# Optimization experiments

Measured on AMD Instinct MI355X. Metric: run time of the kernel, lower is better.

Reference implementation:

```python
import jax, jax.numpy as jnp
import numpy as np

EMBED = 768
NH = 12          # num_heads
NL = 3           # num_levels
NP = 4           # num_points
DV = 384         # value dim = embed_dim * deform_ratio(0.5)
DH = DV // NH    # per-head value dim = 32
B = 16
LQ = 1024        # (512/16)^2 ViT tokens
SHAPES = [(64, 64), (32, 32), (16, 16)]  # 1/8, 1/16, 1/32 pyramid of 512x512
LKV = sum(h * w for h, w in SHAPES)      # 5376
EPS = 1e-6


def layer_norm(x, w, b):
    mu = jnp.mean(x, axis=-1, keepdims=True)
    var = jnp.mean((x - mu) ** 2, axis=-1, keepdims=True)
    return (x - mu) / jnp.sqrt(var + EPS) * w + b


def bilinear_sample(v, loc, H, W):
    # v: (B, NH, H*W, DH); loc: (B, Lq, NH, P, 2) normalized in [0,1]
    # Matches torch grid_sample(align_corners=False, padding_mode='zeros').
    Bv, Lq = loc.shape[0], loc.shape[1]
    x = loc[..., 0] * W - 0.5
    y = loc[..., 1] * H - 0.5
    x0 = jnp.floor(x)
    y0 = jnp.floor(y)
    dx = x - x0
    dy = y - y0
    x0i = x0.astype(jnp.int32)
    y0i = y0.astype(jnp.int32)

    def gather(xi, yi):
        valid = (xi >= 0) & (xi < W) & (yi >= 0) & (yi < H)  # (B,Lq,NH,P)
        xc = jnp.clip(xi, 0, W - 1)
        yc = jnp.clip(yi, 0, H - 1)
        lin = (yc * W + xc).transpose(0, 2, 1, 3).reshape(Bv, NH, Lq * NP)
        g = jnp.take_along_axis(v, lin[..., None], axis=2)  # (B,NH,Lq*P,DH)
        g = g.reshape(Bv, NH, Lq, NP, DH).transpose(0, 2, 1, 3, 4)  # (B,Lq,NH,P,DH)
        return g * valid[..., None].astype(g.dtype)

    g00 = gather(x0i, y0i)
    g01 = gather(x0i + 1, y0i)
    g10 = gather(x0i, y0i + 1)
    g11 = gather(x0i + 1, y0i + 1)
    w00 = ((1 - dx) * (1 - dy))[..., None]
    w01 = (dx * (1 - dy))[..., None]
    w10 = ((1 - dx) * dy)[..., None]
    w11 = (dx * dy)[..., None]
    return g00 * w00 + g01 * w01 + g10 * w10 + g11 * w11


def ms_deform_attn_core(value, shapes_list, loc, aw):
    # value: (B,LKV,NH,DH); loc: (B,Lq,NH,NL,NP,2); aw: (B,Lq,NH,NL,NP)
    Bv, Lq = loc.shape[0], loc.shape[1]
    samples = []
    idx = 0
    for l, (H, W) in enumerate(shapes_list):
        v = value[:, idx:idx + H * W].transpose(0, 2, 1, 3)  # (B,NH,HW,DH)
        idx += H * W
        samples.append(bilinear_sample(v, loc[:, :, :, l], H, W))
    s = jnp.stack(samples, axis=3)  # (B,Lq,NH,NL,NP,DH)
    o = jnp.einsum('bqhlp,bqhlpd->bqhd', aw, s)
    return o.reshape(Bv, Lq, NH * DH)


def setup_inputs() -> dict:
    key = jax.random.key(0)
    ks = jax.random.split(key, 12)

    def n(k, shape, s=0.02):
        return jax.random.normal(k, shape, jnp.float32) * s

    return {
        'q': jax.random.normal(ks[0], (B, LQ, EMBED), jnp.float32),
        'reference_points': jax.random.uniform(ks[1], (B, LQ, NL, 2), jnp.float32),
        'kv': jax.random.normal(ks[2], (B, LKV, EMBED), jnp.float32),
        'spatial_shapes': jnp.asarray(SHAPES, jnp.int32),
        'level_start_index': jnp.asarray(
            np.cumsum([0] + [h * w for h, w in SHAPES])[:-1], jnp.int32),
        'ln1_w': jnp.ones(EMBED, jnp.float32),
        'ln1_b': jnp.zeros(EMBED, jnp.float32),
        'ln2_w': jnp.ones(EMBED, jnp.float32),
        'ln2_b': jnp.zeros(EMBED, jnp.float32),
        'gamma': n(ks[3], (EMBED,), 0.1),
        'w_off': n(ks[4], (EMBED, NH * NL * NP * 2)),
        'b_off': n(ks[5], (NH * NL * NP * 2,), 0.01),
        'w_aw': n(ks[6], (EMBED, NH * NL * NP)),
        'b_aw': jnp.zeros(NH * NL * NP, jnp.float32),
        'w_val': n(ks[7], (EMBED, DV)),
        'b_val': jnp.zeros(DV, jnp.float32),
        'w_out': n(ks[8], (DV, EMBED)),
        'b_out': jnp.zeros(EMBED, jnp.float32),
    }


def reference(q, reference_points, kv, spatial_shapes, level_start_index,
              ln1_w, ln1_b, ln2_w, ln2_b, gamma,
              w_off, b_off, w_aw, b_aw, w_val, b_val, w_out, b_out):
    shapes_list = [tuple(int(v) for v in r) for r in np.asarray(spatial_shapes)]
    Bq, Lq, _ = q.shape
    qn = layer_norm(q, ln1_w, ln1_b)
    kvn = layer_norm(kv, ln2_w, ln2_b)
    value = (kvn @ w_val + b_val).reshape(Bq, -1, NH, DH)
    off = (qn @ w_off + b_off).reshape(Bq, Lq, NH, NL, NP, 2)
    aw = (qn @ w_aw + b_aw).reshape(Bq, Lq, NH, NL * NP)
    aw = jax.nn.softmax(aw, axis=-1).reshape(Bq, Lq, NH, NL, NP)
    # offset normalizer is (W_l, H_l) per level
    wh = jnp.asarray([[w, h] for (h, w) in shapes_list], q.dtype)  # (NL,2)
    loc = reference_points[:, :, None, :, None, :] + off / wh[None, None, None, :, None, :]
    attn = ms_deform_attn_core(value, shapes_list, loc, aw)
    attn = attn @ w_out + b_out
    return q + gamma * attn
```

## Files before the change

kernel.cpp:

```cpp
#include <hip/hip_runtime.h>

#define DEV __device__ __forceinline__

typedef short bf16x8 __attribute__((ext_vector_type(8)));
typedef float f32x4 __attribute__((ext_vector_type(4)));
typedef unsigned int u32;
typedef __attribute__((address_space(1))) const u32* gas_ptr;
typedef __attribute__((address_space(3))) u32* las_ptr;

DEV short f2bf(float f) {
  union { float f; unsigned u; } un; un.f = f;
  unsigned r = un.u + 0x7FFFu + ((un.u >> 16) & 1u);
  return (short)(r >> 16);
}
DEV float bf2f(unsigned short s) {
  union { unsigned u; float f; } un;
  un.u = ((unsigned)s) << 16;
  return un.f;
}
DEV void gload16(const short* g, short* l) {
  __builtin_amdgcn_global_load_lds((gas_ptr)g, (las_ptr)l, 16, 0, 0);
}
DEV float hsum4(float4 v) { return v.x + v.y + v.z + v.w; }

__global__ __launch_bounds__(256) void pack_weights_kernel(
    const float* __restrict__ w_val, const float* __restrict__ w_off,
    const float* __restrict__ w_aw, const float* __restrict__ w_out,
    const float* __restrict__ b_off, const float* __restrict__ b_aw,
    short* __restrict__ wT_val, short* __restrict__ wT_offaw,
    short* __restrict__ wT_out, float* __restrict__ bias_cat) {
  int gid = blockIdx.x * 256 + threadIdx.x;
  const int S0 = 768 * 384, S1 = 768 * 288, S2 = 768 * 144, S3 = 384 * 768;
  const int S4 = 80 * 768, S5 = 512;
  if (gid < S0) { int k = gid / 384, n = gid % 384; wT_val[n * 768 + k] = f2bf(w_val[gid]); return; }
  gid -= S0;
  if (gid < S1) { int k = gid / 288, n = gid % 288; wT_offaw[n * 768 + k] = f2bf(w_off[gid]); return; }
  gid -= S1;
  if (gid < S2) { int k = gid / 144, n = gid % 144; wT_offaw[(288 + n) * 768 + k] = f2bf(w_aw[gid]); return; }
  gid -= S2;
  if (gid < S3) { int k = gid / 768, n = gid % 768; wT_out[n * 384 + k] = f2bf(w_out[gid]); return; }
  gid -= S3;
  if (gid < S4) { wT_offaw[432 * 768 + gid] = 0; return; }
  gid -= S4;
  if (gid < S5) { bias_cat[gid] = (gid < 288) ? b_off[gid] : (gid < 432 ? b_aw[gid - 288] : 0.f); }
}

__global__ __launch_bounds__(256) void ln_norm4_kernel(
    const float* __restrict__ x, const float* __restrict__ w,
    const float* __restrict__ b, short* __restrict__ y) {
  const int wv = threadIdx.x >> 6, lane = threadIdx.x & 63;
  const int row = blockIdx.x * 4 + wv;
  const float* xr = x + (size_t)row * 768;
  float4 v0 = *(const float4*)(xr + lane * 4);
  float4 v1 = *(const float4*)(xr + 256 + lane * 4);
  float4 v2 = *(const float4*)(xr + 512 + lane * 4);
  float s = hsum4(v0) + hsum4(v1) + hsum4(v2);
  #pragma unroll
  for (int off = 32; off > 0; off >>= 1) s += __shfl_xor(s, off, 64);
  const float mu = s * (1.f / 768.f);
  float4 d0 = make_float4(v0.x - mu, v0.y - mu, v0.z - mu, v0.w - mu);
  float4 d1 = make_float4(v1.x - mu, v1.y - mu, v1.z - mu, v1.w - mu);
  float4 d2 = make_float4(v2.x - mu, v2.y - mu, v2.z - mu, v2.w - mu);
  float vs = d0.x * d0.x + d0.y * d0.y + d0.z * d0.z + d0.w * d0.w +
             d1.x * d1.x + d1.y * d1.y + d1.z * d1.z + d1.w * d1.w +
             d2.x * d2.x + d2.y * d2.y + d2.z * d2.z + d2.w * d2.w;
  #pragma unroll
  for (int off = 32; off > 0; off >>= 1) vs += __shfl_xor(vs, off, 64);
  const float rs = rsqrtf(vs * (1.f / 768.f) + 1e-6f);
  const float4 w0 = *(const float4*)(w + lane * 4);
  const float4 w1 = *(const float4*)(w + 256 + lane * 4);
  const float4 w2 = *(const float4*)(w + 512 + lane * 4);
  const float4 b0 = *(const float4*)(b + lane * 4);
  const float4 b1 = *(const float4*)(b + 256 + lane * 4);
  const float4 b2 = *(const float4*)(b + 512 + lane * 4);
  unsigned short* yr = (unsigned short*)y + (size_t)row * 768;
  ushort4 o;
  o.x = (unsigned short)f2bf(d0.x * rs * w0.x + b0.x);
  o.y = (unsigned short)f2bf(d0.y * rs * w0.y + b0.y);
  o.z = (unsigned short)f2bf(d0.z * rs * w0.z + b0.z);
  o.w = (unsigned short)f2bf(d0.w * rs * w0.w + b0.w);
  *(ushort4*)(yr + lane * 4) = o;
  o.x = (unsigned short)f2bf(d1.x * rs * w1.x + b1.x);
  o.y = (unsigned short)f2bf(d1.y * rs * w1.y + b1.y);
  o.z = (unsigned short)f2bf(d1.z * rs * w1.z + b1.z);
  o.w = (unsigned short)f2bf(d1.w * rs * w1.w + b1.w);
  *(ushort4*)(yr + 256 + lane * 4) = o;
  o.x = (unsigned short)f2bf(d2.x * rs * w2.x + b2.x);
  o.y = (unsigned short)f2bf(d2.y * rs * w2.y + b2.y);
  o.z = (unsigned short)f2bf(d2.z * rs * w2.z + b2.z);
  o.w = (unsigned short)f2bf(d2.w * rs * w2.w + b2.w);
  *(ushort4*)(yr + 512 + lane * 4) = o;
}

template <int EMODE>
__global__ __launch_bounds__(256, 3) void gemm128_kernel(
    const short* __restrict__ A, const short* __restrict__ Wt,
    const float* __restrict__ bias, const float* __restrict__ qres,
    const float* __restrict__ gamma, void* __restrict__ Cout,
    const int N, const int K) {
  __shared__ __align__(16) short As[128 * 32];
  __shared__ __align__(16) short Bs[128 * 32];
  const int tid = threadIdx.x;
  const int wave = tid >> 6, lane = tid & 63;

  const int nx = gridDim.x;
  const int id = blockIdx.y * nx + blockIdx.x;
  const int cpx = (nx * gridDim.y) >> 3;
  const int swz = (id & 7) * cpx + (id >> 3);
  const int n0 = (swz % nx) * 128, row0 = (swz / nx) * 128;

  const int lr = lane & 15, quad = lane >> 4;
  const int wm = wave >> 1, wn = wave & 1;

  const short* gA[2]; const short* gB[2];
  #pragma unroll
  for (int rnd = 0; rnd < 2; rnd++) {
    int G = rnd * 256 + wave * 64 + lane;
    int line = G >> 3, pos = G & 7, x = pos ^ (line & 7);
    int r = line * 2 + (x >> 2), qk = (x & 3) * 8;
    gA[rnd] = A + (size_t)(row0 + r) * K + qk;
    gB[rnd] = Wt + (size_t)(n0 + r) * K + qk;
  }
  short* ldsA[2] = {&As[(wave * 64) * 8], &As[(256 + wave * 64) * 8]};
  short* ldsB[2] = {&Bs[(wave * 64) * 8], &Bs[(256 + wave * 64) * 8]};

  const short* aF[4]; const short* bF[4];
  #pragma unroll
  for (int t4 = 0; t4 < 4; t4++) {
    int r = wm * 64 + t4 * 16 + lr;
    int line = r >> 1, pos = ((r & 1) * 4 + quad) ^ (line & 7);
    aF[t4] = &As[(line * 8 + pos) * 8];
    int rb = wn * 64 + t4 * 16 + lr;
    int lineb = rb >> 1, posb = ((rb & 1) * 4 + quad) ^ (lineb & 7);
    bF[t4] = &Bs[(lineb * 8 + posb) * 8];
  }

  f32x4 acc[4][4];
  #pragma unroll
  for (int i = 0; i < 4; i++)
    #pragma unroll
    for (int j = 0; j < 4; j++)
      #pragma unroll
      for (int e = 0; e < 4; e++) acc[i][j][e] = 0.f;

  for (int k0 = 0; k0 < K; k0 += 32) {
    gload16(gA[0], ldsA[0]);
    gload16(gA[1], ldsA[1]);
    gload16(gB[0], ldsB[0]);
    gload16(gB[1], ldsB[1]);
    gA[0] += 32; gA[1] += 32; gB[0] += 32; gB[1] += 32;
    __syncthreads();
    bf16x8 av[4], bv[4];
    #pragma unroll
    for (int t4 = 0; t4 < 4; t4++) {
      av[t4] = *(const bf16x8*)aF[t4];
      bv[t4] = *(const bf16x8*)bF[t4];
    }
    #pragma unroll
    for (int ct = 0; ct < 4; ct++)
      #pragma unroll
      for (int rt = 0; rt < 4; rt++)
        acc[rt][ct] = __builtin_amdgcn_mfma_f32_16x16x32_bf16(av[rt], bv[ct], acc[rt][ct], 0, 0, 0);
    __syncthreads();
  }

  #pragma unroll
  for (int ct = 0; ct < 4; ct++) {
    const int n = n0 + wn * 64 + ct * 16 + lr;
    const float bs = bias[n];
    const float gm = (EMODE == 2) ? gamma[n] : 0.f;
    #pragma unroll
    for (int rt = 0; rt < 4; rt++) {
      #pragma unroll
      for (int i = 0; i < 4; i++) {
        const int m = row0 + wm * 64 + rt * 16 + quad * 4 + i;
        float v = acc[rt][ct][i] + bs;
        if (EMODE == 0) {
          ((short*)Cout)[(size_t)m * N + n] = f2bf(v);
        } else if (EMODE == 1) {
          ((float*)Cout)[(size_t)m * N + n] = v;
        } else {
          ((float*)Cout)[(size_t)m * N + n] = qres[(size_t)m * N + n] + gm * v;
        }
      }
    }
  }
}

__global__ __launch_bounds__(384) void sampler_kernel(
    const float* __restrict__ offaw,
    const float* __restrict__ refp,
    const short* __restrict__ value,
    short* __restrict__ o) {
  const int tid = threadIdx.x;
  const int qi = tid / 96, t = tid % 96;
  const int head = t >> 3, ln4 = t & 7;
  const int bq = blockIdx.x * 4 + qi;
  __shared__ __align__(16) float s[4][440];
  __shared__ float sref[4][6];
  const float* row = offaw + (size_t)bq * 512;
  #pragma unroll
  for (int i = t; i < 108; i += 96)
    *(float4*)&s[qi][i * 4] = *(const float4*)&row[i * 4];
  if (t < 6) sref[qi][t] = refp[(size_t)bq * 6 + t];
  __syncthreads();

  const float* awp = &s[qi][288 + head * 12];
  float mx = awp[0];
  #pragma unroll
  for (int j = 1; j < 12; j++) mx = fmaxf(mx, awp[j]);
  float wgt[12];
  float ssum = 0.f;
  #pragma unroll
  for (int j = 0; j < 12; j++) { float e = __expf(awp[j] - mx); wgt[j] = e; ssum += e; }
  const float inv = 1.f / ssum;

  const int b = bq >> 10;
  const unsigned short* vb =
      (const unsigned short*)value + (size_t)b * 5376 * 384 + head * 32 + ln4 * 4;
  float4 acc = make_float4(0.f, 0.f, 0.f, 0.f);
  const int HW[3] = {64, 32, 16};
  const int starts[3] = {0, 4096, 5120};
  #pragma unroll
  for (int l = 0; l < 3; l++) {
    const int Wi = HW[l];
    const float Wf = (float)Wi;
    const float rx = sref[qi][l * 2], ry = sref[qi][l * 2 + 1];
    const unsigned short* base = vb + (size_t)starts[l] * 384;
    #pragma unroll
    for (int p = 0; p < 4; p++) {
      const int oi = ((head * 3 + l) * 4 + p) * 2;
      float x = fmaf(rx, Wf, s[qi][oi] - 0.5f);
      float y = fmaf(ry, Wf, s[qi][oi + 1] - 0.5f);
      float xf = floorf(x), yf = floorf(y);
      float dx = x - xf, dy = y - yf;
      int x0 = (int)xf, y0 = (int)yf;
      int x1 = x0 + 1, y1 = y0 + 1;
      int x0c = min(max(x0, 0), Wi - 1), x1c = min(max(x1, 0), Wi - 1);
      int y0c = min(max(y0, 0), Wi - 1), y1c = min(max(y1, 0), Wi - 1);
      float wx0 = (x0 >= 0 && x0 < Wi) ? (1.f - dx) : 0.f;
      float wx1 = (x1 < Wi && x1 >= 0) ? dx : 0.f;
      float wy0 = (y0 >= 0 && y0 < Wi) ? (1.f - dy) : 0.f;
      float wy1 = (y1 < Wi && y1 >= 0) ? dy : 0.f;
      const ushort4 u00 = *(const ushort4*)(base + (size_t)(y0c * Wi + x0c) * 384);
      const ushort4 u01 = *(const ushort4*)(base + (size_t)(y0c * Wi + x1c) * 384);
      const ushort4 u10 = *(const ushort4*)(base + (size_t)(y1c * Wi + x0c) * 384);
      const ushort4 u11 = *(const ushort4*)(base + (size_t)(y1c * Wi + x1c) * 384);
      const float w00 = wx0 * wy0, w01 = wx1 * wy0, w10 = wx0 * wy1, w11 = wx1 * wy1;
      const float g = wgt[l * 4 + p];
      acc.x += g * (w00 * bf2f(u00.x) + w01 * bf2f(u01.x) + w10 * bf2f(u10.x) + w11 * bf2f(u11.x));
      acc.y += g * (w00 * bf2f(u00.y) + w01 * bf2f(u01.y) + w10 * bf2f(u10.y) + w11 * bf2f(u11.y));
      acc.z += g * (w00 * bf2f(u00.z) + w01 * bf2f(u01.z) + w10 * bf2f(u10.z) + w11 * bf2f(u11.z));
      acc.w += g * (w00 * bf2f(u00.w) + w01 * bf2f(u01.w) + w10 * bf2f(u10.w) + w11 * bf2f(u11.w));
    }
  }
  ushort4 outv;
  outv.x = (unsigned short)f2bf(acc.x * inv);
  outv.y = (unsigned short)f2bf(acc.y * inv);
  outv.z = (unsigned short)f2bf(acc.z * inv);
  outv.w = (unsigned short)f2bf(acc.w * inv);
  *(ushort4*)((unsigned short*)o + (size_t)bq * 384 + head * 32 + ln4 * 4) = outv;
}

extern "C" void kernel_launch(void* const* d_in, const int* in_sizes, int n_in,
                              void* d_out, int out_size, void* d_ws, size_t ws_size,
                              hipStream_t stream) {
  (void)in_sizes; (void)n_in; (void)out_size; (void)ws_size;
  const float* q     = (const float*)d_in[0];
  const float* refp  = (const float*)d_in[1];
  const float* kv    = (const float*)d_in[2];
  const float* ln1w  = (const float*)d_in[5];
  const float* ln1b  = (const float*)d_in[6];
  const float* ln2w  = (const float*)d_in[7];
  const float* ln2b  = (const float*)d_in[8];
  const float* gamma = (const float*)d_in[9];
  const float* w_off = (const float*)d_in[10];
  const float* b_off = (const float*)d_in[11];
  const float* w_aw  = (const float*)d_in[12];
  const float* b_aw  = (const float*)d_in[13];
  const float* w_val = (const float*)d_in[14];
  const float* b_val = (const float*)d_in[15];
  const float* w_out = (const float*)d_in[16];
  const float* b_out = (const float*)d_in[17];
  float* out = (float*)d_out;

  char* wsp = (char*)d_ws;
  size_t cur = 0;
  auto alloc = [&](size_t bytes) -> void* {
    cur = (cur + 255) & ~(size_t)255;
    void* p = wsp + cur;
    cur += bytes;
    return p;
  };
  short*  wT_val   = (short*)alloc((size_t)384 * 768 * 2);
  short*  wT_offaw = (short*)alloc((size_t)512 * 768 * 2);
  short*  wT_out   = (short*)alloc((size_t)768 * 384 * 2);
  float*  bias_cat = (float*)alloc((size_t)512 * 4);
  short*  kvn      = (short*)alloc((size_t)86016 * 768 * 2);
  short*  qn       = (short*)alloc((size_t)16384 * 768 * 2);
  short*  value    = (short*)alloc((size_t)86016 * 384 * 2);
  float*  offaw    = (float*)alloc((size_t)16384 * 512 * 4);
  short*  obuf     = (short*)alloc((size_t)16384 * 384 * 2);

  pack_weights_kernel<<<3842, 256, 0, stream>>>(w_val, w_off, w_aw, w_out, b_off,
                                                b_aw, wT_val, wT_offaw, wT_out,
                                                bias_cat);
  ln_norm4_kernel<<<21504, 256, 0, stream>>>(kv, ln2w, ln2b, kvn);
  ln_norm4_kernel<<<4096, 256, 0, stream>>>(q, ln1w, ln1b, qn);
  gemm128_kernel<0><<<dim3(3, 672), 256, 0, stream>>>(
      kvn, wT_val, b_val, nullptr, nullptr, value, 384, 768);
  gemm128_kernel<1><<<dim3(4, 128), 256, 0, stream>>>(
      qn, wT_offaw, bias_cat, nullptr, nullptr, offaw, 512, 768);
  sampler_kernel<<<4096, 384, 0, stream>>>(offaw, refp, value, obuf);
  gemm128_kernel<2><<<dim3(6, 128), 256, 0, stream>>>(
      obuf, wT_out, b_out, q, gamma, out, 768, 384);
}
```

Before: 665.8 us.

## Double GEMM K-tile to 64 and remap sampler block order

The GEMM kernel now stages a 128x64 K-slab per iteration into enlarged LDS tiles, using a new swizzled layout. Each barrier pair is followed by two MFMA sub-steps, which halves the number of __syncthreads per K. Separately, the sampler kernel remaps blockIdx with a stride-8 permutation so adjacent blocks spread differently, presumably to align with XCD scheduling. The GEMM costs twice the LDS, which may reduce occupancy. The sampler remap hardcodes 4096 blocks.

```diff
diff --git a/kernel.cpp b/kernel.cpp
--- a/kernel.cpp
+++ b/kernel.cpp
@@ -98,8 +98,8 @@
     const float* __restrict__ bias, const float* __restrict__ qres,
     const float* __restrict__ gamma, void* __restrict__ Cout,
     const int N, const int K) {
-  __shared__ __align__(16) short As[128 * 32];
-  __shared__ __align__(16) short Bs[128 * 32];
+  __shared__ __align__(16) short As[128 * 64];
+  __shared__ __align__(16) short Bs[128 * 64];
   const int tid = threadIdx.x;
   const int wave = tid >> 6, lane = tid & 63;
 
@@ -112,27 +112,30 @@
   const int lr = lane & 15, quad = lane >> 4;
   const int wm = wave >> 1, wn = wave & 1;
 
-  const short* gA[2]; const short* gB[2];
-  #pragma unroll
-  for (int rnd = 0; rnd < 2; rnd++) {
+  const short* gA[4]; const short* gB[4];
+  short* ldsA[4]; short* ldsB[4];
+  #pragma unroll
+  for (int rnd = 0; rnd < 4; rnd++) {
     int G = rnd * 256 + wave * 64 + lane;
     int line = G >> 3, pos = G & 7, x = pos ^ (line & 7);
-    int r = line * 2 + (x >> 2), qk = (x & 3) * 8;
-    gA[rnd] = A + (size_t)(row0 + r) * K + qk;
-    gB[rnd] = Wt + (size_t)(n0 + r) * K + qk;
-  }
-  short* ldsA[2] = {&As[(wave * 64) * 8], &As[(256 + wave * 64) * 8]};
-  short* ldsB[2] = {&Bs[(wave * 64) * 8], &Bs[(256 + wave * 64) * 8]};
-
-  const short* aF[4]; const short* bF[4];
-  #pragma unroll
-  for (int t4 = 0; t4 < 4; t4++) {
-    int r = wm * 64 + t4 * 16 + lr;
-    int line = r >> 1, pos = ((r & 1) * 4 + quad) ^ (line & 7);
-    aF[t4] = &As[(line * 8 + pos) * 8];
-    int rb = wn * 64 + t4 * 16 + lr;
-    int lineb = rb >> 1, posb = ((rb & 1) * 4 + quad) ^ (lineb & 7);
-    bF[t4] = &Bs[(lineb * 8 + posb) * 8];
+    gA[rnd] = A + (size_t)(row0 + line) * K + x * 8;
+    gB[rnd] = Wt + (size_t)(n0 + line) * K + x * 8;
+    ldsA[rnd] = &As[(rnd * 256 + wave * 64) * 8];
+    ldsB[rnd] = &Bs[(rnd * 256 + wave * 64) * 8];
+  }
+
+  const short* aF[2][4]; const short* bF[2][4];
+  #pragma unroll
+  for (int ks = 0; ks < 2; ks++) {
+    #pragma unroll
+    for (int t4 = 0; t4 < 4; t4++) {
+      int r = wm * 64 + t4 * 16 + lr;
+      int pos = (ks * 4 + quad) ^ (r & 7);
+      aF[ks][t4] = &As[(r * 8 + pos) * 8];
+      int rb = wn * 64 + t4 * 16 + lr;
+      int posb = (ks * 4 + quad) ^ (rb & 7);
+      bF[ks][t4] = &Bs[(rb * 8 + posb) * 8];
+    }
   }
 
   f32x4 acc[4][4];
@@ -143,24 +146,28 @@
       #pragma unroll
       for (int e = 0; e < 4; e++) acc[i][j][e] = 0.f;
 
-  for (int k0 = 0; k0 < K; k0 += 32) {
-    gload16(gA[0], ldsA[0]);
-    gload16(gA[1], ldsA[1]);
-    gload16(gB[0], ldsB[0]);
-    gload16(gB[1], ldsB[1]);
-    gA[0] += 32; gA[1] += 32; gB[0] += 32; gB[1] += 32;
+  for (int k0 = 0; k0 < K; k0 += 64) {
+    #pragma unroll
+    for (int rnd = 0; rnd < 4; rnd++) gload16(gA[rnd], ldsA[rnd]);
+    #pragma unroll
+    for (int rnd = 0; rnd < 4; rnd++) gload16(gB[rnd], ldsB[rnd]);
+    #pragma unroll
+    for (int rnd = 0; rnd < 4; rnd++) { gA[rnd] += 64; gB[rnd] += 64; }
     __syncthreads();
-    bf16x8 av[4], bv[4];
-    #pragma unroll
-    for (int t4 = 0; t4 < 4; t4++) {
-      av[t4] = *(const bf16x8*)aF[t4];
-      bv[t4] = *(const bf16x8*)bF[t4];
+    #pragma unroll
+    for (int ks = 0; ks < 2; ks++) {
+      bf16x8 av[4], bv[4];
+      #pragma unroll
+      for (int t4 = 0; t4 < 4; t4++) {
+        av[t4] = *(const bf16x8*)aF[ks][t4];
+        bv[t4] = *(const bf16x8*)bF[ks][t4];
+      }
+      #pragma unroll
+      for (int ct = 0; ct < 4; ct++)
+        #pragma unroll
+        for (int rt = 0; rt < 4; rt++)
+          acc[rt][ct] = __builtin_amdgcn_mfma_f32_16x16x32_bf16(av[rt], bv[ct], acc[rt][ct], 0, 0, 0);
     }
-    #pragma unroll
-    for (int ct = 0; ct < 4; ct++)
-      #pragma unroll
-      for (int rt = 0; rt < 4; rt++)
-        acc[rt][ct] = __builtin_amdgcn_mfma_f32_16x16x32_bf16(av[rt], bv[ct], acc[rt][ct], 0, 0, 0);
     __syncthreads();
   }
 
@@ -195,7 +202,8 @@
   const int tid = threadIdx.x;
   const int qi = tid / 96, t = tid % 96;
   const int head = t >> 3, ln4 = t & 7;
-  const int bq = blockIdx.x * 4 + qi;
+  const int blk = (blockIdx.x & 7) * 512 + (blockIdx.x >> 3);
+  const int bq = blk * 4 + qi;
   __shared__ __align__(16) float s[4][440];
   __shared__ float sref[4][6];
   const float* row = offaw + (size_t)bq * 512;
```

Result: faster. 651.0 us (-2.2%).
